# Kernel optimization log

Measured on AMD Instinct MI355X. Metric: run time of the kernel, lower is better.

The kernel has to match this reference:

```python
import jax, jax.numpy as jnp
import numpy as np

N = 10000
E = 320000

def leaky(x):
    return jnp.where(x >= 0, x, 0.01 * x)

def spmm(rows, cols, vals, dense):
    # sparse(N,N) @ dense(N,D) via gather + segment-sum
    return jax.ops.segment_sum(vals[:, None] * dense[cols], rows, num_segments=N)

def setup_inputs() -> dict:
    key = jax.random.key(0)
    ks = jax.random.split(key, 16)
    def xav(k, shp):
        std = float(np.sqrt(2.0 / (shp[0] + shp[1])))
        return jax.random.normal(k, shp, dtype=jnp.float32) * std
    return {
        "x": jax.random.normal(ks[0], (N, 512), dtype=jnp.float32),
        "adj_rows": jax.random.randint(ks[1], (E,), 0, N, dtype=jnp.int32),
        "adj_cols": jax.random.randint(ks[2], (E,), 0, N, dtype=jnp.int32),
        "adj_vals": jax.random.uniform(ks[3], (E,), dtype=jnp.float32),
        "W1": xav(ks[4], (512, 256)), "b1": jnp.zeros((256,), jnp.float32),
        "Wc1a": xav(ks[5], (256, 128)), "bc1a": jnp.zeros((128,), jnp.float32),
        "Wc1b": xav(ks[6], (128, 64)), "bc1b": jnp.zeros((64,), jnp.float32),
        "Wc2a": xav(ks[7], (64, 128)), "bc2a": jnp.zeros((128,), jnp.float32),
        "Wc2b": xav(ks[8], (128, 256)), "bc2b": jnp.zeros((256,), jnp.float32),
        "W6": xav(ks[9], (256, 512)), "b6": jnp.zeros((512,), jnp.float32),
    }

def reference(x, adj_rows, adj_cols, adj_vals, W1, b1, Wc1a, bc1a, Wc1b, bc1b,
              Wc2a, bc2a, Wc2b, bc2b, W6, b6):
    # encode (eval mode: dropout is identity)
    h = spmm(adj_rows, adj_cols, adj_vals, x @ W1) + b1   # gc1
    h = leaky(h)
    z = leaky(h @ Wc1a + bc1a) @ Wc1b + bc1b              # classifier1, [N,64]
    # inner-product decoder with identity activation -> dense NxN adjacency
    A = z @ z.T                                            # [N,N]
    # decode: classifier2 then gc6 applied with the DENSE reconstructed adj
    h2 = leaky(z @ Wc2a + bc2a) @ Wc2b + bc2b              # [N,256]
    h2 = leaky(h2)
    out = A @ (h2 @ W6) + b6                               # [N,512]
    return (out, z)
```

## Files before the change

### kernel.cpp

```cpp
#include <hip/hip_runtime.h>
#include <hip/hip_bf16.h>

#define NROWS 10000
#define KPAD  10240

typedef __attribute__((ext_vector_type(8))) short bf16x8;
typedef __attribute__((ext_vector_type(4))) float f32x4;

__device__ __forceinline__ float leaky_f(float x) { return x >= 0.f ? x : 0.01f * x; }

__device__ __forceinline__ unsigned short f2bf(float f) {
    union { float f; unsigned int u; } v; v.f = f;
    unsigned int r = v.u + 0x7fffu + ((v.u >> 16) & 1u);
    return (unsigned short)(r >> 16);
}
__device__ __forceinline__ float bf2f(unsigned short h) {
    union { unsigned int u; float f; } v; v.u = ((unsigned int)h) << 16;
    return v.f;
}

__global__ void conv_all(const float* __restrict__ x, const float* __restrict__ W1,
                         const float* __restrict__ Wc1a, const float* __restrict__ Wc1b,
                         const float* __restrict__ Wc2a, const float* __restrict__ Wc2b,
                         const float* __restrict__ W6,
                         unsigned short* __restrict__ XHI,
                         unsigned short* __restrict__ o1, unsigned short* __restrict__ o2,
                         unsigned short* __restrict__ o3, unsigned short* __restrict__ o4,
                         unsigned short* __restrict__ o5, unsigned short* __restrict__ o6,
                         int* __restrict__ counts, unsigned short* __restrict__ Zt,
                         unsigned short* __restrict__ H2t) {
    int gid = blockIdx.x * 256 + threadIdx.x;
    if (gid < 1280000) {
        float4 v = ((const float4*)x)[gid];
        ushort4 h;
        h.x = f2bf(v.x); h.y = f2bf(v.y); h.z = f2bf(v.z); h.w = f2bf(v.w);
        ((ushort4*)XHI)[gid] = h;
    } else if (gid < 1411072) {
        int i = gid - 1280000, k = i >> 8, n = i & 255;
        o1[n * 512 + k] = f2bf(W1[i]);
    } else if (gid < 1443840) {
        int i = gid - 1411072, k = i >> 7, n = i & 127;
        o2[n * 256 + k] = f2bf(Wc1a[i]);
    } else if (gid < 1452032) {
        int i = gid - 1443840, k = i >> 6, n = i & 63;
        o3[n * 128 + k] = f2bf(Wc1b[i]);
    } else if (gid < 1460224) {
        int i = gid - 1452032, k = i >> 7, n = i & 127;
        o4[n * 64 + k] = f2bf(Wc2a[i]);
    } else if (gid < 1492992) {
        int i = gid - 1460224, k = i >> 8, n = i & 255;
        o5[n * 128 + k] = f2bf(Wc2b[i]);
    } else if (gid < 1624064) {
        int i = gid - 1492992, k = i >> 9, n = i & 511;
        o6[n * 256 + k] = f2bf(W6[i]);
    } else if (gid < 1634064) {
        counts[gid - 1624064] = 0;
    } else if (gid < 1649424) {
        int i = gid - 1634064;
        Zt[(size_t)(i / 240) * KPAD + 10000 + (i % 240)] = 0;
    } else if (gid < 1710864) {
        int i = gid - 1649424;
        H2t[(size_t)(i / 240) * KPAD + 10000 + (i % 240)] = 0;
    }
}

__global__ void hist_kernel(const int* __restrict__ rows, int* __restrict__ counts, int E) {
    int i = blockIdx.x * blockDim.x + threadIdx.x;
    if (i < E) atomicAdd(&counts[rows[i]], 1);
}

__global__ __launch_bounds__(1024)
void scan_kernel(const int* __restrict__ counts, int* __restrict__ starts,
                 int* __restrict__ cursor, int n) {
    __shared__ int buf[1024];
    int tid = threadIdx.x;
    int base = tid * 10;
    int v[10];
    int local = 0;
#pragma unroll
    for (int j = 0; j < 10; ++j) {
        int i = base + j;
        v[j] = (i < n) ? counts[i] : 0;
        local += v[j];
    }
    buf[tid] = local;
    __syncthreads();
    for (int off = 1; off < 1024; off <<= 1) {
        int t = (tid >= off) ? buf[tid - off] : 0;
        __syncthreads();
        buf[tid] += t;
        __syncthreads();
    }
    int run = buf[tid] - local;
#pragma unroll
    for (int j = 0; j < 10; ++j) {
        int i = base + j;
        if (i < n) { starts[i] = run; cursor[i] = run; run += v[j]; }
    }
    if (tid == 1023) starts[n] = buf[1023];
}

__global__ void scatter_kernel(const int* __restrict__ rows, const int* __restrict__ cols,
                               const float* __restrict__ vals, int* __restrict__ cursor,
                               int* __restrict__ cols_s, float* __restrict__ vals_s, int E) {
    int i = blockIdx.x * blockDim.x + threadIdx.x;
    if (i < E) {
        int pos = atomicAdd(&cursor[rows[i]], 1);
        cols_s[pos] = cols[i];
        vals_s[pos] = vals[i];
    }
}

__global__ __launch_bounds__(64)
void spmm_leaky_half(const int* __restrict__ starts, const int* __restrict__ cols_s,
                     const float* __restrict__ vals_s, const unsigned short* __restrict__ C1b,
                     const float* __restrict__ b1, unsigned short* __restrict__ Hb) {
    int r = blockIdx.x;
    int cbase = blockIdx.y * 128 + threadIdx.x * 2;
    float a0x = b1[cbase], a0y = b1[cbase + 1];
    float a1x = 0.f, a1y = 0.f, a2x = 0.f, a2y = 0.f, a3x = 0.f, a3y = 0.f;
    int s = starts[r], e = starts[r + 1];
    int p = s;
    for (; p + 4 <= e; p += 4) {
        int c0 = cols_s[p], c1 = cols_s[p + 1], c2 = cols_s[p + 2], c3 = cols_s[p + 3];
        float v0 = vals_s[p], v1 = vals_s[p + 1], v2 = vals_s[p + 2], v3 = vals_s[p + 3];
        ushort2 s0 = *(const ushort2*)(C1b + (size_t)c0 * 256 + cbase);
        ushort2 s1 = *(const ushort2*)(C1b + (size_t)c1 * 256 + cbase);
        ushort2 s2 = *(const ushort2*)(C1b + (size_t)c2 * 256 + cbase);
        ushort2 s3 = *(const ushort2*)(C1b + (size_t)c3 * 256 + cbase);
        a0x += v0 * bf2f(s0.x); a0y += v0 * bf2f(s0.y);
        a1x += v1 * bf2f(s1.x); a1y += v1 * bf2f(s1.y);
        a2x += v2 * bf2f(s2.x); a2y += v2 * bf2f(s2.y);
        a3x += v3 * bf2f(s3.x); a3y += v3 * bf2f(s3.y);
    }
    for (; p < e; ++p) {
        int c0 = cols_s[p];
        float v0 = vals_s[p];
        ushort2 s0 = *(const ushort2*)(C1b + (size_t)c0 * 256 + cbase);
        a0x += v0 * bf2f(s0.x); a0y += v0 * bf2f(s0.y);
    }
    ushort2 h;
    h.x = f2bf(leaky_f(a0x + a1x + a2x + a3x));
    h.y = f2bf(leaky_f(a0y + a1y + a2y + a3y));
    *(ushort2*)(Hb + (size_t)r * 256 + cbase) = h;
}

template<int ACT, int WF32, int WBF, int WTB>
__global__ __launch_bounds__(256)
void gemm_mfma(const unsigned short* __restrict__ A, const unsigned short* __restrict__ Bt,
               const float* __restrict__ bias, float* __restrict__ Cf,
               unsigned short* __restrict__ Cb, unsigned short* __restrict__ Ct,
               int ldt, int M, int N, int K) {
    __shared__ short sA[64][72];
    __shared__ short sB[64][72];
    const int bm = blockIdx.x * 64;
    const int bn = blockIdx.y * 64;
    const int tid = threadIdx.x;
    const int lane = tid & 63, wid = tid >> 6;
    const int wm = wid & 1, wn = wid >> 1;
    const int l15 = lane & 15, kg = lane >> 4;

    f32x4 acc[2][2];
#pragma unroll
    for (int i = 0; i < 2; i++)
#pragma unroll
        for (int j = 0; j < 2; j++) acc[i][j] = (f32x4){0.f, 0.f, 0.f, 0.f};

    for (int k0 = 0; k0 < K; k0 += 64) {
#pragma unroll
        for (int it = 0; it < 2; ++it) {
            int idx = tid + it * 256;
            int r = idx >> 3, s = idx & 7;
            int gm = bm + r;
            uint4 va = {0u, 0u, 0u, 0u};
            if (gm < M) va = *(const uint4*)(A + (size_t)gm * K + k0 + s * 8);
            *(uint4*)(&sA[r][s * 8]) = va;
            uint4 vb = *(const uint4*)(Bt + (size_t)(bn + r) * K + k0 + s * 8);
            *(uint4*)(&sB[r][s * 8]) = vb;
        }
        __syncthreads();
        bf16x8 a[2][2], b[2][2];
#pragma unroll
        for (int i = 0; i < 2; i++)
#pragma unroll
            for (int ks = 0; ks < 2; ++ks) {
                a[i][ks] = *(const bf16x8*)(&sA[wm * 32 + i * 16 + l15][kg * 8 + ks * 32]);
                b[i][ks] = *(const bf16x8*)(&sB[wn * 32 + i * 16 + l15][kg * 8 + ks * 32]);
            }
#pragma unroll
        for (int ks = 0; ks < 2; ++ks)
#pragma unroll
            for (int i = 0; i < 2; i++)
#pragma unroll
                for (int j = 0; j < 2; j++)
                    acc[i][j] = __builtin_amdgcn_mfma_f32_16x16x32_bf16(a[i][ks], b[j][ks], acc[i][j], 0, 0, 0);
        __syncthreads();
    }

#pragma unroll
    for (int i = 0; i < 2; i++) {
        int row0 = wm * 32 + i * 16 + kg * 4;
#pragma unroll
        for (int j = 0; j < 2; j++) {
            int col = bn + wn * 32 + j * 16 + l15;
            float bv = bias ? bias[col] : 0.f;
            ushort4 tw;
#pragma unroll
            for (int r = 0; r < 4; r++) {
                int grow = bm + row0 + r;
                float v = acc[i][j][r] + bv;
                if (ACT) v = leaky_f(v);
                if (WF32) { if (grow < M) Cf[(size_t)grow * N + col] = v; }
                if (WBF)  { if (grow < M) Cb[(size_t)grow * N + col] = f2bf(v); }
                if (WTB)  ((unsigned short*)&tw)[r] = f2bf(v);
            }
            if (WTB && (bm + row0) < M)
                *(ushort4*)(&Ct[(size_t)col * ldt + bm + row0]) = tw;
        }
    }
}

__global__ __launch_bounds__(256)
void fused_enc(const unsigned short* __restrict__ H,
               const unsigned short* __restrict__ Wa,
               const unsigned short* __restrict__ Wb,
               const float* __restrict__ ba, const float* __restrict__ bb,
               float* __restrict__ Zf, unsigned short* __restrict__ Zb,
               unsigned short* __restrict__ Zt, int M) {
    __shared__ short sA[64][72];
    __shared__ short sB[128][72];
    __shared__ short sT1[64][136];
    __shared__ short sWb[64][136];
    const int bm = blockIdx.x * 64;
    const int tid = threadIdx.x;
    const int lane = tid & 63, wid = tid >> 6;
    const int wm = wid & 1, wn = wid >> 1;
    const int l15 = lane & 15, kg = lane >> 4;

#pragma unroll
    for (int it = 0; it < 4; ++it) {
        int idx = tid + it * 256;
        int r = idx >> 4, s = idx & 15;
        *(uint4*)(&sWb[r][s * 8]) = *(const uint4*)(Wb + r * 128 + s * 8);
    }

    f32x4 accA[2][4];
#pragma unroll
    for (int i = 0; i < 2; i++)
#pragma unroll
        for (int j = 0; j < 4; j++) accA[i][j] = (f32x4){0.f, 0.f, 0.f, 0.f};

    for (int k0 = 0; k0 < 256; k0 += 64) {
#pragma unroll
        for (int it = 0; it < 2; ++it) {
            int idx = tid + it * 256;
            int r = idx >> 3, s = idx & 7;
            int gm = bm + r;
            uint4 va = {0u, 0u, 0u, 0u};
            if (gm < M) va = *(const uint4*)(H + (size_t)gm * 256 + k0 + s * 8);
            *(uint4*)(&sA[r][s * 8]) = va;
        }
#pragma unroll
        for (int it = 0; it < 4; ++it) {
            int idx = tid + it * 256;
            int r = idx >> 3, s = idx & 7;
            *(uint4*)(&sB[r][s * 8]) = *(const uint4*)(Wa + r * 256 + k0 + s * 8);
        }
        __syncthreads();
#pragma unroll
        for (int ks = 0; ks < 2; ++ks) {
            bf16x8 a[2], b[4];
#pragma unroll
            for (int i = 0; i < 2; i++)
                a[i] = *(const bf16x8*)(&sA[wm * 32 + i * 16 + l15][kg * 8 + ks * 32]);
#pragma unroll
            for (int j = 0; j < 4; j++)
                b[j] = *(const bf16x8*)(&sB[wn * 64 + j * 16 + l15][kg * 8 + ks * 32]);
#pragma unroll
            for (int i = 0; i < 2; i++)
#pragma unroll
                for (int j = 0; j < 4; j++)
                    accA[i][j] = __builtin_amdgcn_mfma_f32_16x16x32_bf16(a[i], b[j], accA[i][j], 0, 0, 0);
        }
        __syncthreads();
    }
#pragma unroll
    for (int i = 0; i < 2; i++) {
        int row0 = wm * 32 + i * 16 + kg * 4;
#pragma unroll
        for (int j = 0; j < 4; j++) {
            int col = wn * 64 + j * 16 + l15;
            float bv = ba[col];
#pragma unroll
            for (int r = 0; r < 4; r++)
                sT1[row0 + r][col] = f2bf(leaky_f(accA[i][j][r] + bv));
        }
    }
    __syncthreads();

    f32x4 accB[2][2];
#pragma unroll
    for (int i = 0; i < 2; i++)
#pragma unroll
        for (int j = 0; j < 2; j++) accB[i][j] = (f32x4){0.f, 0.f, 0.f, 0.f};
#pragma unroll
    for (int kc = 0; kc < 4; ++kc) {
        bf16x8 a[2], b[2];
#pragma unroll
        for (int i = 0; i < 2; i++)
            a[i] = *(const bf16x8*)(&sT1[wm * 32 + i * 16 + l15][kc * 32 + kg * 8]);
#pragma unroll
        for (int j = 0; j < 2; j++)
            b[j] = *(const bf16x8*)(&sWb[wn * 32 + j * 16 + l15][kc * 32 + kg * 8]);
#pragma unroll
        for (int i = 0; i < 2; i++)
#pragma unroll
            for (int j = 0; j < 2; j++)
                accB[i][j] = __builtin_amdgcn_mfma_f32_16x16x32_bf16(a[i], b[j], accB[i][j], 0, 0, 0);
    }
#pragma unroll
    for (int i = 0; i < 2; i++) {
        int row0 = wm * 32 + i * 16 + kg * 4;
#pragma unroll
        for (int j = 0; j < 2; j++) {
            int col = wn * 32 + j * 16 + l15;
            float bv = bb[col];
            ushort4 tw;
#pragma unroll
            for (int r = 0; r < 4; r++) {
                int grow = bm + row0 + r;
                float v = accB[i][j][r] + bv;
                if (grow < M) {
                    Zf[(size_t)grow * 64 + col] = v;
                    Zb[(size_t)grow * 64 + col] = f2bf(v);
                }
                ((unsigned short*)&tw)[r] = f2bf(v);
            }
            if ((bm + row0) < M)
                *(ushort4*)(&Zt[(size_t)col * KPAD + bm + row0]) = tw;
        }
    }
}

__global__ __launch_bounds__(256)
void fused_dec(const unsigned short* __restrict__ Z,
               const unsigned short* __restrict__ Wa,
               const unsigned short* __restrict__ Wb,
               const float* __restrict__ ba, const float* __restrict__ bb,
               unsigned short* __restrict__ H2t, int M) {
    __shared__ short sA[64][72];
    __shared__ short sB[128][72];
    __shared__ short sT2[64][136];
    __shared__ short sB2[256][72];
    const int bm = blockIdx.x * 64;
    const int tid = threadIdx.x;
    const int lane = tid & 63, wid = tid >> 6;
    const int wm = wid & 1, wn = wid >> 1;
    const int l15 = lane & 15, kg = lane >> 4;

#pragma unroll
    for (int it = 0; it < 2; ++it) {
        int idx = tid + it * 256;
        int r = idx >> 3, s = idx & 7;
        int gm = bm + r;
        uint4 va = {0u, 0u, 0u, 0u};
        if (gm < M) va = *(const uint4*)(Z + (size_t)gm * 64 + s * 8);
        *(uint4*)(&sA[r][s * 8]) = va;
    }
#pragma unroll
    for (int it = 0; it < 4; ++it) {
        int idx = tid + it * 256;
        int r = idx >> 3, s = idx & 7;
        *(uint4*)(&sB[r][s * 8]) = *(const uint4*)(Wa + r * 64 + s * 8);
    }
    __syncthreads();
    f32x4 accA[2][4];
#pragma unroll
    for (int i = 0; i < 2; i++)
#pragma unroll
        for (int j = 0; j < 4; j++) accA[i][j] = (f32x4){0.f, 0.f, 0.f, 0.f};
#pragma unroll
    for (int ks = 0; ks < 2; ++ks) {
        bf16x8 a[2], b[4];
#pragma unroll
        for (int i = 0; i < 2; i++)
            a[i] = *(const bf16x8*)(&sA[wm * 32 + i * 16 + l15][kg * 8 + ks * 32]);
#pragma unroll
        for (int j = 0; j < 4; j++)
            b[j] = *(const bf16x8*)(&sB[wn * 64 + j * 16 + l15][kg * 8 + ks * 32]);
#pragma unroll
        for (int i = 0; i < 2; i++)
#pragma unroll
            for (int j = 0; j < 4; j++)
                accA[i][j] = __builtin_amdgcn_mfma_f32_16x16x32_bf16(a[i], b[j], accA[i][j], 0, 0, 0);
    }
    __syncthreads();
#pragma unroll
    for (int i = 0; i < 2; i++) {
        int row0 = wm * 32 + i * 16 + kg * 4;
#pragma unroll
        for (int j = 0; j < 4; j++) {
            int col = wn * 64 + j * 16 + l15;
            float bv = ba[col];
#pragma unroll
            for (int r = 0; r < 4; r++)
                sT2[row0 + r][col] = f2bf(leaky_f(accA[i][j][r] + bv));
        }
    }
    __syncthreads();

    f32x4 accB[2][8];
#pragma unroll
    for (int i = 0; i < 2; i++)
#pragma unroll
        for (int j = 0; j < 8; j++) accB[i][j] = (f32x4){0.f, 0.f, 0.f, 0.f};
    for (int k0 = 0; k0 < 128; k0 += 64) {
#pragma unroll
        for (int it = 0; it < 8; ++it) {
            int idx = tid + it * 256;
            int r = idx >> 3, s = idx & 7;
            *(uint4*)(&sB2[r][s * 8]) = *(const uint4*)(Wb + r * 128 + k0 + s * 8);
        }
        __syncthreads();
#pragma unroll
        for (int ks = 0; ks < 2; ++ks) {
            bf16x8 a[2], b[8];
#pragma unroll
            for (int i = 0; i < 2; i++)
                a[i] = *(const bf16x8*)(&sT2[wm * 32 + i * 16 + l15][k0 + ks * 32 + kg * 8]);
#pragma unroll
            for (int j = 0; j < 8; j++)
                b[j] = *(const bf16x8*)(&sB2[wn * 128 + j * 16 + l15][kg * 8 + ks * 32]);
#pragma unroll
            for (int i = 0; i < 2; i++)
#pragma unroll
                for (int j = 0; j < 8; j++)
                    accB[i][j] = __builtin_amdgcn_mfma_f32_16x16x32_bf16(a[i], b[j], accB[i][j], 0, 0, 0);
        }
        __syncthreads();
    }
#pragma unroll
    for (int i = 0; i < 2; i++) {
        int row0 = wm * 32 + i * 16 + kg * 4;
#pragma unroll
        for (int j = 0; j < 8; j++) {
            int col = wn * 128 + j * 16 + l15;
            float bv = bb[col];
            ushort4 tw;
#pragma unroll
            for (int r = 0; r < 4; r++)
                ((unsigned short*)&tw)[r] = f2bf(leaky_f(accB[i][j][r] + bv));
            if ((bm + row0) < M)
                *(ushort4*)(&H2t[(size_t)col * KPAD + bm + row0]) = tw;
        }
    }
}

__global__ __launch_bounds__(256)
void sgemm_sk(const unsigned short* __restrict__ Zt, const unsigned short* __restrict__ H2t,
              float* __restrict__ part) {
    __shared__ short sA[64][72];
    __shared__ short sB[64][72];
    const int bn = blockIdx.x * 64;
    const int kc = blockIdx.y;
    const int tid = threadIdx.x;
    const int lane = tid & 63, wid = tid >> 6;
    const int wm = wid & 1, wn = wid >> 1;
    const int l15 = lane & 15, kg = lane >> 4;

    f32x4 acc[2][2];
#pragma unroll
    for (int i = 0; i < 2; i++)
#pragma unroll
        for (int j = 0; j < 2; j++) acc[i][j] = (f32x4){0.f, 0.f, 0.f, 0.f};

    for (int kk = 0; kk < 4; ++kk) {
        int k0 = kc * 256 + kk * 64;
#pragma unroll
        for (int it = 0; it < 2; ++it) {
            int idx = tid + it * 256;
            int r = idx >> 3, s = idx & 7;
            *(uint4*)(&sA[r][s * 8]) = *(const uint4*)(Zt + (size_t)r * KPAD + k0 + s * 8);
            *(uint4*)(&sB[r][s * 8]) = *(const uint4*)(H2t + (size_t)(bn + r) * KPAD + k0 + s * 8);
        }
        __syncthreads();
        bf16x8 a[2][2], b[2][2];
#pragma unroll
        for (int i = 0; i < 2; i++)
#pragma unroll
            for (int ks = 0; ks < 2; ++ks) {
                a[i][ks] = *(const bf16x8*)(&sA[wm * 32 + i * 16 + l15][kg * 8 + ks * 32]);
                b[i][ks] = *(const bf16x8*)(&sB[wn * 32 + i * 16 + l15][kg * 8 + ks * 32]);
            }
#pragma unroll
        for (int ks = 0; ks < 2; ++ks)
#pragma unroll
            for (int i = 0; i < 2; i++)
#pragma unroll
                for (int j = 0; j < 2; j++)
                    acc[i][j] = __builtin_amdgcn_mfma_f32_16x16x32_bf16(a[i][ks], b[j][ks], acc[i][j], 0, 0, 0);
        __syncthreads();
    }
#pragma unroll
    for (int i = 0; i < 2; i++) {
        int row0 = wm * 32 + i * 16 + kg * 4;
#pragma unroll
        for (int j = 0; j < 2; j++) {
            int col = bn + wn * 32 + j * 16 + l15;
#pragma unroll
            for (int r = 0; r < 4; r++)
                part[((size_t)kc * 64 + row0 + r) * 256 + col] = acc[i][j][r];
        }
    }
}

__global__ void reduce_S2(const float* __restrict__ part, unsigned short* __restrict__ S2b) {
    int i = blockIdx.x * blockDim.x + threadIdx.x;
    if (i < 64 * 256) {
        float s = 0.f;
#pragma unroll
        for (int c = 0; c < 40; ++c) s += part[(size_t)c * (64 * 256) + i];
        S2b[i] = f2bf(s);
    }
}

extern "C" void kernel_launch(void* const* d_in, const int* in_sizes, int n_in,
                              void* d_out, int out_size, void* d_ws, size_t ws_size,
                              hipStream_t stream) {
    const float* x    = (const float*)d_in[0];
    const int*   rows = (const int*)d_in[1];
    const int*   cols = (const int*)d_in[2];
    const float* vals = (const float*)d_in[3];
    const float* W1   = (const float*)d_in[4];
    const float* b1   = (const float*)d_in[5];
    const float* Wc1a = (const float*)d_in[6];
    const float* bc1a = (const float*)d_in[7];
    const float* Wc1b = (const float*)d_in[8];
    const float* bc1b = (const float*)d_in[9];
    const float* Wc2a = (const float*)d_in[10];
    const float* bc2a = (const float*)d_in[11];
    const float* Wc2b = (const float*)d_in[12];
    const float* bc2b = (const float*)d_in[13];
    const float* W6   = (const float*)d_in[14];
    const float* b6   = (const float*)d_in[15];

    const int N = NROWS;
    const int E = in_sizes[1];

    float* ws = (float*)d_ws;
    unsigned short* XHI  = (unsigned short*)(ws + 0);
    unsigned short* C1b  = (unsigned short*)(ws + 2560000);
    unsigned short* HHI  = (unsigned short*)(ws + 3840000);
    unsigned short* ZHI  = (unsigned short*)(ws + 5120000);
    unsigned short* ZT   = (unsigned short*)(ws + 5440000);
    unsigned short* H2T  = (unsigned short*)(ws + 5767680);
    float*          PART = ws + 7078400;
    unsigned short* S2B  = (unsigned short*)(ws + 7733760);
    unsigned short* W6ST = (unsigned short*)(ws + 7741952);
    unsigned short* W1T   = (unsigned short*)(ws + 7758336);
    unsigned short* WC1AT = (unsigned short*)(ws + 7823872);
    unsigned short* WC1BT = (unsigned short*)(ws + 7840256);
    unsigned short* WC2AT = (unsigned short*)(ws + 7844352);
    unsigned short* WC2BT = (unsigned short*)(ws + 7848448);
    unsigned short* W6T   = (unsigned short*)(ws + 7864832);

    int*   counts = (int*)(ws + 7930368);
    int*   starts = counts + 10000;
    int*   cursor = starts + 10001;
    int*   cols_s = cursor + 10000;
    float* vals_s = (float*)(cols_s + 320000);

    float* Out = (float*)d_out;
    float* Zp  = (float*)d_out + 5120000;

    const int GX = (N + 63) / 64;

    conv_all<<<6683, 256, 0, stream>>>(x, W1, Wc1a, Wc1b, Wc2a, Wc2b, W6, XHI,
                                       W1T, WC1AT, WC1BT, WC2AT, WC2BT, W6T,
                                       counts, ZT, H2T);

    hist_kernel<<<(E + 255) / 256, 256, 0, stream>>>(rows, counts, E);
    scan_kernel<<<1, 1024, 0, stream>>>(counts, starts, cursor, N);
    scatter_kernel<<<(E + 255) / 256, 256, 0, stream>>>(rows, cols, vals, cursor, cols_s, vals_s, E);

    gemm_mfma<0,0,1,0><<<dim3(GX, 4), 256, 0, stream>>>(XHI, W1T, nullptr,
                                                        nullptr, C1b, nullptr, 0, N, 256, 512);

    spmm_leaky_half<<<dim3(N, 2), 64, 0, stream>>>(starts, cols_s, vals_s, C1b, b1, HHI);

    fused_enc<<<GX, 256, 0, stream>>>(HHI, WC1AT, WC1BT, bc1a, bc1b, Zp, ZHI, ZT, N);

    fused_dec<<<GX, 256, 0, stream>>>(ZHI, WC2AT, WC2BT, bc2a, bc2b, H2T, N);

    sgemm_sk<<<dim3(4, 40), 256, 0, stream>>>(ZT, H2T, PART);
    reduce_S2<<<64, 256, 0, stream>>>(PART, S2B);

    gemm_mfma<0,0,0,1><<<dim3(1, 8), 256, 0, stream>>>(S2B, W6T, nullptr,
                                                       nullptr, nullptr, W6ST, 64, 64, 512, 256);

    gemm_mfma<0,1,0,0><<<dim3(GX, 8), 256, 0, stream>>>(ZHI, W6ST, b6,
                                                        Out, nullptr, nullptr, 0, N, 512, 64);
}
```

Measured before the change: 137.0 us.

## Pack CSR edges as int2 and widen SpMM gathers to 16-byte loads

The scatter step now stores each sorted edge's column and value together as one int2, so one load fetches both. The SpMM kernel now uses one 64-thread block per row instead of two. Each half-wave handles alternate edges and gathers 8 bf16 features per lane with a 16-byte load, then the halves are combined with a cross-half shuffle before bias, leaky and store. This cuts the number of load instructions and edge-metadata fetches, but gives half as many blocks and leaves half the threads idle during the final write.

```diff
diff --git a/kernel.cpp b/kernel.cpp
--- a/kernel.cpp
+++ b/kernel.cpp
@@ -102,47 +102,84 @@
 
 __global__ void scatter_kernel(const int* __restrict__ rows, const int* __restrict__ cols,
                                const float* __restrict__ vals, int* __restrict__ cursor,
-                               int* __restrict__ cols_s, float* __restrict__ vals_s, int E) {
+                               int2* __restrict__ edge_s, int E) {
     int i = blockIdx.x * blockDim.x + threadIdx.x;
     if (i < E) {
         int pos = atomicAdd(&cursor[rows[i]], 1);
-        cols_s[pos] = cols[i];
-        vals_s[pos] = vals[i];
+        edge_s[pos] = make_int2(cols[i], __float_as_int(vals[i]));
     }
 }
 
 __global__ __launch_bounds__(64)
-void spmm_leaky_half(const int* __restrict__ starts, const int* __restrict__ cols_s,
-                     const float* __restrict__ vals_s, const unsigned short* __restrict__ C1b,
-                     const float* __restrict__ b1, unsigned short* __restrict__ Hb) {
+void spmm_leaky_w2(const int* __restrict__ starts, const int2* __restrict__ edge_s,
+                   const unsigned short* __restrict__ C1b, const float* __restrict__ b1,
+                   unsigned short* __restrict__ Hb) {
     int r = blockIdx.x;
-    int cbase = blockIdx.y * 128 + threadIdx.x * 2;
-    float a0x = b1[cbase], a0y = b1[cbase + 1];
-    float a1x = 0.f, a1y = 0.f, a2x = 0.f, a2y = 0.f, a3x = 0.f, a3y = 0.f;
+    int half = threadIdx.x >> 5;
+    int l32 = threadIdx.x & 31;
+    int cbase = l32 * 8;
+    float a0[8], a1[8];
+#pragma unroll
+    for (int j = 0; j < 8; ++j) { a0[j] = 0.f; a1[j] = 0.f; }
     int s = starts[r], e = starts[r + 1];
-    int p = s;
-    for (; p + 4 <= e; p += 4) {
-        int c0 = cols_s[p], c1 = cols_s[p + 1], c2 = cols_s[p + 2], c3 = cols_s[p + 3];
-        float v0 = vals_s[p], v1 = vals_s[p + 1], v2 = vals_s[p + 2], v3 = vals_s[p + 3];
-        ushort2 s0 = *(const ushort2*)(C1b + (size_t)c0 * 256 + cbase);
-        ushort2 s1 = *(const ushort2*)(C1b + (size_t)c1 * 256 + cbase);
-        ushort2 s2 = *(const ushort2*)(C1b + (size_t)c2 * 256 + cbase);
-        ushort2 s3 = *(const ushort2*)(C1b + (size_t)c3 * 256 + cbase);
-        a0x += v0 * bf2f(s0.x); a0y += v0 * bf2f(s0.y);
-        a1x += v1 * bf2f(s1.x); a1y += v1 * bf2f(s1.y);
-        a2x += v2 * bf2f(s2.x); a2y += v2 * bf2f(s2.y);
-        a3x += v3 * bf2f(s3.x); a3y += v3 * bf2f(s3.y);
-    }
-    for (; p < e; ++p) {
-        int c0 = cols_s[p];
-        float v0 = vals_s[p];
-        ushort2 s0 = *(const ushort2*)(C1b + (size_t)c0 * 256 + cbase);
-        a0x += v0 * bf2f(s0.x); a0y += v0 * bf2f(s0.y);
-    }
-    ushort2 h;
-    h.x = f2bf(leaky_f(a0x + a1x + a2x + a3x));
-    h.y = f2bf(leaky_f(a0y + a1y + a2y + a3y));
-    *(ushort2*)(Hb + (size_t)r * 256 + cbase) = h;
+    int p = s + half;
+    for (; p + 2 < e; p += 4) {
+        int2 e0 = edge_s[p];
+        int2 e1 = edge_s[p + 2];
+        float v0 = __int_as_float(e0.y);
+        float v1 = __int_as_float(e1.y);
+        uint4 q0 = *(const uint4*)(C1b + (size_t)e0.x * 256 + cbase);
+        uint4 q1 = *(const uint4*)(C1b + (size_t)e1.x * 256 + cbase);
+        a0[0] += v0 * bf2f((unsigned short)(q0.x & 0xffff));
+        a0[1] += v0 * bf2f((unsigned short)(q0.x >> 16));
+        a0[2] += v0 * bf2f((unsigned short)(q0.y & 0xffff));
+        a0[3] += v0 * bf2f((unsigned short)(q0.y >> 16));
+        a0[4] += v0 * bf2f((unsigned short)(q0.z & 0xffff));
+        a0[5] += v0 * bf2f((unsigned short)(q0.z >> 16));
+        a0[6] += v0 * bf2f((unsigned short)(q0.w & 0xffff));
+        a0[7] += v0 * bf2f((unsigned short)(q0.w >> 16));
+        a1[0] += v1 * bf2f((unsigned short)(q1.x & 0xffff));
+        a1[1] += v1 * bf2f((unsigned short)(q1.x >> 16));
+        a1[2] += v1 * bf2f((unsigned short)(q1.y & 0xffff));
+        a1[3] += v1 * bf2f((unsigned short)(q1.y >> 16));
+        a1[4] += v1 * bf2f((unsigned short)(q1.z & 0xffff));
+        a1[5] += v1 * bf2f((unsigned short)(q1.z >> 16));
+        a1[6] += v1 * bf2f((unsigned short)(q1.w & 0xffff));
+        a1[7] += v1 * bf2f((unsigned short)(q1.w >> 16));
+    }
+    if (p < e) {
+        int2 e0 = edge_s[p];
+        float v0 = __int_as_float(e0.y);
+        uint4 q0 = *(const uint4*)(C1b + (size_t)e0.x * 256 + cbase);
+        a0[0] += v0 * bf2f((unsigned short)(q0.x & 0xffff));
+        a0[1] += v0 * bf2f((unsigned short)(q0.x >> 16));
+        a0[2] += v0 * bf2f((unsigned short)(q0.y & 0xffff));
+        a0[3] += v0 * bf2f((unsigned short)(q0.y >> 16));
+        a0[4] += v0 * bf2f((unsigned short)(q0.z & 0xffff));
+        a0[5] += v0 * bf2f((unsigned short)(q0.z >> 16));
+        a0[6] += v0 * bf2f((unsigned short)(q0.w & 0xffff));
+        a0[7] += v0 * bf2f((unsigned short)(q0.w >> 16));
+    }
+    float f[8];
+#pragma unroll
+    for (int j = 0; j < 8; ++j) {
+        float v = a0[j] + a1[j];
+        v += __shfl_xor(v, 32);
+        f[j] = v;
+    }
+    if (half == 0) {
+        uint4 h;
+        unsigned int w0 = (unsigned int)f2bf(leaky_f(f[0] + b1[cbase + 0]))
+                        | ((unsigned int)f2bf(leaky_f(f[1] + b1[cbase + 1])) << 16);
+        unsigned int w1 = (unsigned int)f2bf(leaky_f(f[2] + b1[cbase + 2]))
+                        | ((unsigned int)f2bf(leaky_f(f[3] + b1[cbase + 3])) << 16);
+        unsigned int w2 = (unsigned int)f2bf(leaky_f(f[4] + b1[cbase + 4]))
+                        | ((unsigned int)f2bf(leaky_f(f[5] + b1[cbase + 5])) << 16);
+        unsigned int w3 = (unsigned int)f2bf(leaky_f(f[6] + b1[cbase + 6]))
+                        | ((unsigned int)f2bf(leaky_f(f[7] + b1[cbase + 7])) << 16);
+        h.x = w0; h.y = w1; h.z = w2; h.w = w3;
+        *(uint4*)(Hb + (size_t)r * 256 + cbase) = h;
+    }
 }
 
 template<int ACT, int WF32, int WBF, int WTB>
@@ -567,8 +604,7 @@
     int*   counts = (int*)(ws + 7930368);
     int*   starts = counts + 10000;
     int*   cursor = starts + 10001;
-    int*   cols_s = cursor + 10000;
-    float* vals_s = (float*)(cols_s + 320000);
+    int2*  edge_s = (int2*)(cursor + 10000);
 
     float* Out = (float*)d_out;
     float* Zp  = (float*)d_out + 5120000;
@@ -581,12 +617,12 @@
 
     hist_kernel<<<(E + 255) / 256, 256, 0, stream>>>(rows, counts, E);
     scan_kernel<<<1, 1024, 0, stream>>>(counts, starts, cursor, N);
-    scatter_kernel<<<(E + 255) / 256, 256, 0, stream>>>(rows, cols, vals, cursor, cols_s, vals_s, E);
+    scatter_kernel<<<(E + 255) / 256, 256, 0, stream>>>(rows, cols, vals, cursor, edge_s, E);
 
     gemm_mfma<0,0,1,0><<<dim3(GX, 4), 256, 0, stream>>>(XHI, W1T, nullptr,
                                                         nullptr, C1b, nullptr, 0, N, 256, 512);
 
-    spmm_leaky_half<<<dim3(N, 2), 64, 0, stream>>>(starts, cols_s, vals_s, C1b, b1, HHI);
+    spmm_leaky_w2<<<N, 64, 0, stream>>>(starts, edge_s, C1b, b1, HHI);
 
     fused_enc<<<GX, 256, 0, stream>>>(HHI, WC1AT, WC1BT, bc1a, bc1b, Zp, ZHI, ZT, N);
 
```

After: 138.9 us. About the same (+1.4%).
